# Kernel optimization log

Hardware: AMD Instinct MI355X
Metric: run time of the kernel (lower is better)

Reference implementation:

```python
import jax, jax.numpy as jnp
import numpy as np

D, M, B, K = 512, 128, 16, 4
COHERENCE_COEFF = 0.01
LAMBDA_COEFF = 1.0


def setup_inputs() -> dict:
    key = jax.random.key(0)
    k1, k2, k3, k4 = jax.random.split(key, 4)
    x = jax.random.normal(k1, (2, 2048, D), dtype=jnp.float32)
    V = jax.random.normal(k2, (D, M, B), dtype=jnp.float32)
    U = jax.random.normal(k3, (M, D, B), dtype=jnp.float32)
    u_scales = jax.random.normal(k4, (M, B), dtype=jnp.float32)
    return {"x": x, "V": V, "U": U, "u_scales": u_scales}


def _forward(x, V, U, u_scales):
    # UnitColNorm parametrizations: normalize over the D axis
    Vn = V / jnp.linalg.norm(V, axis=0, keepdims=True)          # (D, m, b)
    Un = U / jnp.linalg.norm(U, axis=1, keepdims=True)          # (m, D, b)
    s = jnp.tanh(u_scales) * LAMBDA_COEFF                        # (m, b)
    U_eff = Un * s[:, None, :]                                   # (m, D, b)

    expert_reprs = jnp.einsum('...d,dmb->...mb', x, Vn)          # (..., m, b)
    repr_l2_sq = jnp.sum(expert_reprs * expert_reprs, axis=-1)   # (..., m)
    topk_vals, topk_idxs = jax.lax.top_k(repr_l2_sq, K)          # (..., k)

    reprs_topk = jnp.take_along_axis(expert_reprs, topk_idxs[..., None], axis=-2)  # (..., k, b)
    U_active = U_eff[topk_idxs]                                  # (..., k, D, b)
    writes = jnp.einsum('...kdb,...kb->...d', U_active, reprs_topk)

    # aux terms
    N = topk_vals.size // K
    idxs_flat = topk_idxs.reshape(-1)
    vals_flat = topk_vals.reshape(-1)
    energy_per_expert = jnp.zeros((M,), dtype=vals_flat.dtype).at[idxs_flat].add(vals_flat) / N
    select_rate = jnp.zeros((M,), dtype=vals_flat.dtype).at[idxs_flat].add(1.0) / N
    total_energy = jnp.maximum(energy_per_expert.sum(), 1e-12)
    relative_energy = energy_per_expert / total_energy

    eye = jnp.eye(M * B, dtype=Vn.dtype)
    sqrtD = jnp.sqrt(jnp.asarray(D, dtype=Vn.dtype))

    def coherence_penalty(Mtx):
        G = Mtx.T @ Mtx  # (m*b, m*b)
        return jnp.abs(G - eye).mean() * sqrtD

    v_pen = coherence_penalty(Vn.reshape(D, M * B))
    u_pen = coherence_penalty(U_eff.transpose(1, 0, 2).reshape(D, M * B))
    aux_loss = COHERENCE_COEFF * v_pen - total_energy

    out = x + writes
    return (out, total_energy, energy_per_expert, relative_energy,
            select_rate, v_pen, u_pen, aux_loss)


def reference(x, V, U, u_scales):
    return _forward(x, V, U, u_scales)
```

## Files before the change

kernel.cpp:

```cpp
#include <hip/hip_runtime.h>
#include <math.h>

#define D 512
#define M 128
#define B 16
#define KSEL 4
#define NC 2048
#define NTOK 4096

typedef unsigned short ushort;
typedef unsigned int uint;
typedef unsigned long long u64;
typedef __attribute__((ext_vector_type(8))) short short8;
typedef __attribute__((ext_vector_type(4))) float floatx4;

#define WS_EACC   0
#define WS_CACC   128
#define WS_VSUM   256
#define WS_USUM   257
#define WS_CNT_I  258
#define WS_VSCALE 512
#define WS_USCALE 2560
#define WS_E_F    4608
#define WS_RBF_F  528896
#define WS_XH_F   2626048
#define WS_XL_F   3674624
#define WS_VHT_F  4723200
#define WS_VLT_F  5247488
#define WS_UHT_F  5771776
#define WS_ULT_F  6296064
#define WS_LIST_F 6820352

#define OUT_TE   2097152
#define OUT_EPE  2097153
#define OUT_RE   2097281
#define OUT_SR   2097409
#define OUT_VPEN 2097537
#define OUT_UPEN 2097538
#define OUT_AUX  2097539

#define GLDS16(g, l) __builtin_amdgcn_global_load_lds(                        \
    (const __attribute__((address_space(1))) unsigned int*)(g),               \
    (__attribute__((address_space(3))) unsigned int*)(l), 16, 0, 0)

__device__ __forceinline__ ushort f2bf(float f) {
    union { float f; uint u; } a; a.f = f;
    uint u = a.u;
    u += 0x7fffu + ((u >> 16) & 1u);
    return (ushort)(u >> 16);
}
__device__ __forceinline__ float bf2f(ushort h) {
    union { uint u; float f; } a; a.u = ((uint)h) << 16;
    return a.f;
}

__launch_bounds__(256)
__global__ void prep_kernel(const float* __restrict__ x, const float* __restrict__ V,
                            const float* __restrict__ U, const float* __restrict__ us_in,
                            ushort* __restrict__ xh, ushort* __restrict__ xl,
                            ushort* __restrict__ vht, ushort* __restrict__ vlt,
                            ushort* __restrict__ uht, ushort* __restrict__ ult,
                            float* __restrict__ ws) {
    __shared__ float ts[64][65];
    const int bid = blockIdx.x;
    const int tid = threadIdx.x;

    if (bid < 1024) {
        const int idx = (bid * 256 + tid) * 8;
        float4 v0 = *(const float4*)(x + idx);
        float4 v1 = *(const float4*)(x + idx + 4);
        float vv[8] = {v0.x, v0.y, v0.z, v0.w, v1.x, v1.y, v1.z, v1.w};
        union { ushort u[8]; uint4 q; } H, L;
#pragma unroll
        for (int j = 0; j < 8; ++j) {
            ushort h = f2bf(vv[j]);
            H.u[j] = h;
            L.u[j] = f2bf(vv[j] - bf2f(h));
        }
        *(uint4*)(xh + idx) = H.q;
        *(uint4*)(xl + idx) = L.q;
    } else if (bid < 1280) {
        const int vb = bid - 1024;
        const int col0 = (vb & 31) * 64;
        const int d0 = (vb >> 5) * 64;
#pragma unroll
        for (int i = 0; i < 16; ++i) {
            int idx = i * 256 + tid;
            int r = idx >> 6, c = idx & 63;
            ts[r][c] = V[(size_t)(d0 + r) * NC + col0 + c];
        }
        __syncthreads();
#pragma unroll
        for (int i = 0; i < 16; ++i) {
            int idx = i * 256 + tid;
            int c2 = idx >> 6, d2 = idx & 63;
            float v = ts[d2][c2];
            ushort h = f2bf(v);
            vht[(size_t)(col0 + c2) * D + d0 + d2] = h;
            vlt[(size_t)(col0 + c2) * D + d0 + d2] = f2bf(v - bf2f(h));
        }
    } else if (bid < 1408) {
        const int m = bid - 1280;
        float (*t2)[129] = (float (*)[129])ts;
        for (int d0 = 0; d0 < D; d0 += 128) {
            __syncthreads();
#pragma unroll
            for (int i = 0; i < 8; ++i) {
                int idx = i * 256 + tid;
                int d2 = idx >> 4, b2 = idx & 15;
                t2[b2][d2] = U[(size_t)m * (D * B) + (size_t)(d0 + d2) * B + b2];
            }
            __syncthreads();
#pragma unroll
            for (int i = 0; i < 8; ++i) {
                int idx = i * 256 + tid;
                int b3 = idx >> 7, d3 = idx & 127;
                float v = t2[b3][d3];
                ushort h = f2bf(v);
                uht[(size_t)((m << 4) + b3) * D + d0 + d3] = h;
                ult[(size_t)((m << 4) + b3) * D + d0 + d3] = f2bf(v - bf2f(h));
            }
        }
    } else {
        const int bx = bid - 1408;
        if (bx >= 160) {
            ws[(bx - 160) * 256 + tid] = 0.0f;
            return;
        }
        if (bx < 32) {
            const int c = bx * 64 + (tid & 63);
            const int dg = tid >> 6;
            float s = 0.0f;
            for (int d = dg; d < D; d += 4) {
                float v = V[(size_t)d * NC + c];
                s = fmaf(v, v, s);
            }
            float (*sh)[64] = (float (*)[64])ts;
            sh[dg][tid & 63] = s;
            __syncthreads();
            if (tid < 64) {
                float t = (sh[0][tid] + sh[1][tid]) + (sh[2][tid] + sh[3][tid]);
                ws[WS_VSCALE + bx * 64 + tid] = 1.0f / sqrtf(t);
            }
        } else {
            const int m = bx - 32;
            const float* p = U + (size_t)m * (D * B);
            float s = 0.0f;
            for (int i = tid; i < D * B; i += 256) {
                float v = p[i];
                s = fmaf(v, v, s);
            }
            float* sh2 = &ts[0][0];
            sh2[tid] = s;
            __syncthreads();
            if (tid < 16) {
                float t = 0.0f;
#pragma unroll
                for (int j = 0; j < 16; ++j) t += sh2[tid + (j << 4)];
                ws[WS_USCALE + (m << 4) + tid] = tanhf(us_in[(m << 4) + tid]) / sqrtf(t);
            }
        }
    }
}

__launch_bounds__(256)
__global__ void mfma_fused(const ushort* __restrict__ xh, const ushort* __restrict__ xl,
                           const ushort* __restrict__ vht, const ushort* __restrict__ vlt,
                           const ushort* __restrict__ uht, const ushort* __restrict__ ult,
                           float* __restrict__ ws, ushort* __restrict__ rbf) {
    __shared__ ushort smem[16384];
    const int bid = blockIdx.x;
    const int tid = threadIdx.x, lane = tid & 63, w = tid >> 6;
    const int wr = w >> 1, wc = w & 1;
    const int r15 = lane & 15, q = lane >> 4;
    const int srl = lane >> 2;
    const int skq = (lane & 3) ^ ((lane >> 3) & 3);
    const int perm8 = (q ^ ((r15 >> 1) & 3)) * 8;

    const int is_gemm = bid < 512;
    const ushort* srcs[4];
    int rbase[4];
    int gi = 0, gj = 0, which = 0;
    if (is_gemm) {
        const int x = bid & 7, inner = bid >> 3;
        const int tokG = ((x >> 1) << 3) + (inner & 7);
        const int colG = ((x & 1) << 3) + (inner >> 3);
        const int tokB = tokG * 128, colB = colG * 128;
        srcs[0] = xh; srcs[1] = xl; srcs[2] = vht; srcs[3] = vlt;
        rbase[0] = tokB; rbase[1] = tokB; rbase[2] = colB; rbase[3] = colB;
    } else {
        int t = bid - 512;
        which = t >= 136;
        if (which) t -= 136;
        int bi = 0, rem = 16;
        while (t >= rem) { t -= rem; --rem; ++bi; }
        gi = bi; gj = bi + t;
        const ushort* ht = which ? uht : vht;
        srcs[0] = ht; srcs[1] = ht; srcs[2] = ht; srcs[3] = ht;
        rbase[0] = gi * 128; rbase[1] = gi * 128; rbase[2] = gj * 128; rbase[3] = gj * 128;
    }

    floatx4 acc[4][4];
#pragma unroll
    for (int i = 0; i < 4; ++i)
#pragma unroll
        for (int j = 0; j < 4; ++j) acc[i][j] = (floatx4){0.f, 0.f, 0.f, 0.f};

    auto stage = [&](int c) {
        const int kb = c * 32 + skq * 8;
#pragma unroll
        for (int tI = 0; tI < 4; ++tI) {
            if (!is_gemm && (tI & 1)) continue;
            const ushort* s = srcs[tI] + (size_t)rbase[tI] * D + kb;
#pragma unroll
            for (int sub = 0; sub < 2; ++sub) {
                const int row16 = w * 32 + sub * 16;
                GLDS16(s + (size_t)(row16 + srl) * D,
                       &smem[tI * 4096 + row16 * 32]);
            }
        }
    };

    stage(0);
    for (int c = 0; c < 16; ++c) {
        __syncthreads();
        short8 ah[4], al[4], bh[4], bl[4];
#pragma unroll
        for (int s = 0; s < 4; ++s) {
            const int ra = (wr * 64 + s * 16 + r15) * 32 + perm8;
            ah[s] = *(const short8*)&smem[ra];
            const int rb = (wc * 64 + s * 16 + r15) * 32 + perm8;
            bh[s] = *(const short8*)&smem[8192 + rb];
            if (is_gemm) {
                al[s] = *(const short8*)&smem[4096 + ra];
                bl[s] = *(const short8*)&smem[12288 + rb];
            }
        }
        __syncthreads();
        if (c < 15) stage(c + 1);
#pragma unroll
        for (int st = 0; st < 4; ++st)
#pragma unroll
            for (int sc = 0; sc < 4; ++sc) {
                acc[st][sc] = __builtin_amdgcn_mfma_f32_16x16x32_bf16(ah[st], bh[sc], acc[st][sc], 0, 0, 0);
                if (is_gemm) {
                    acc[st][sc] = __builtin_amdgcn_mfma_f32_16x16x32_bf16(ah[st], bl[sc], acc[st][sc], 0, 0, 0);
                    acc[st][sc] = __builtin_amdgcn_mfma_f32_16x16x32_bf16(al[st], bh[sc], acc[st][sc], 0, 0, 0);
                }
            }
    }

    if (is_gemm) {
        const int tok0 = rbase[0] + wr * 64, col0 = rbase[2] + wc * 64;
        const int cg4 = col0 >> 6;
        float* e2base = ws + WS_E_F + (size_t)cg4 * (NTOK * 4);
#pragma unroll
        for (int st = 0; st < 4; ++st) {
            const int rowb = tok0 + st * 16 + q * 4;
            float er[4][4];
#pragma unroll
            for (int sc = 0; sc < 4; ++sc) {
                const int colg = col0 + sc * 16 + r15;
                const float vs = ws[WS_VSCALE + colg];
                float r0 = acc[st][sc][0] * vs;
                float r1 = acc[st][sc][1] * vs;
                float r2 = acc[st][sc][2] * vs;
                float r3 = acc[st][sc][3] * vs;
                rbf[(size_t)(rowb + 0) * NC + colg] = f2bf(r0);
                rbf[(size_t)(rowb + 1) * NC + colg] = f2bf(r1);
                rbf[(size_t)(rowb + 2) * NC + colg] = f2bf(r2);
                rbf[(size_t)(rowb + 3) * NC + colg] = f2bf(r3);
                float e0 = r0 * r0, e1 = r1 * r1, e2 = r2 * r2, e3 = r3 * r3;
#pragma unroll
                for (int mk = 1; mk < 16; mk <<= 1) {
                    e0 += __shfl_xor(e0, mk);
                    e1 += __shfl_xor(e1, mk);
                    e2 += __shfl_xor(e2, mk);
                    e3 += __shfl_xor(e3, mk);
                }
                er[sc][0] = e0; er[sc][1] = e1; er[sc][2] = e2; er[sc][3] = e3;
            }
            if (r15 == 0) {
#pragma unroll
                for (int j = 0; j < 4; ++j) {
                    *(float4*)(e2base + (size_t)(rowb + j) * 4) =
                        make_float4(er[0][j], er[1][j], er[2][j], er[3][j]);
                }
            }
        }
    } else {
        const float* scl = ws + (which ? WS_USCALE : WS_VSCALE);
        float* sum_out = ws + (which ? WS_USUM : WS_VSUM);
        float local = 0.0f;
#pragma unroll
        for (int sc = 0; sc < 4; ++sc) {
            const int colg = gj * 128 + wc * 64 + sc * 16 + r15;
            const float scj = scl[colg];
#pragma unroll
            for (int st = 0; st < 4; ++st) {
#pragma unroll
                for (int reg = 0; reg < 4; ++reg) {
                    const int rowg = gi * 128 + wr * 64 + st * 16 + q * 4 + reg;
                    float g = acc[st][sc][reg] * scl[rowg] * scj;
                    if (rowg == colg) g -= 1.0f;
                    local += fabsf(g);
                }
            }
        }
        if (gi < gj) local *= 2.0f;
#pragma unroll
        for (int mk = 1; mk < 64; mk <<= 1) local += __shfl_xor(local, mk);
        __shared__ float red[4];
        if (lane == 0) red[w] = local;
        __syncthreads();
        if (tid == 0) atomicAdd(sum_out, (red[0] + red[1]) + (red[2] + red[3]));
    }
}

__launch_bounds__(256)
__global__ void topk_kernel(float* __restrict__ ws) {
    const int tid = threadIdx.x, lane = tid & 63, w = tid >> 6;
    const int t = blockIdx.x * 4 + w;
    int* icnt = (int*)ws + WS_CNT_I;
    int* ilist = (int*)(ws + WS_LIST_F);

    const int cg4 = lane >> 1;
    const int e2off = (lane & 1) * 2;
    const float2 ev = *(const float2*)(ws + WS_E_F +
                                       ((size_t)cg4 * NTOK + t) * 4 + e2off);
    const uint i0 = (uint)(lane * 2), i1 = i0 + 1;
    u64 k0 = ((u64)__float_as_uint(ev.x) << 32) | (uint)(~i0);
    u64 k1 = ((u64)__float_as_uint(ev.y) << 32) | (uint)(~i1);
    u64 s0 = k0 > k1 ? k0 : k1;
    u64 s1 = k0 > k1 ? k1 : k0;
    u64 s2 = 0, s3 = 0;

#pragma unroll
    for (int mk = 1; mk < 64; mk <<= 1) {
        u64 o0 = __shfl_xor(s0, mk);
        u64 o1 = __shfl_xor(s1, mk);
        u64 o2 = __shfl_xor(s2, mk);
        u64 o3 = __shfl_xor(s3, mk);
        u64 c0 = s0 > o3 ? s0 : o3;
        u64 c1 = s1 > o2 ? s1 : o2;
        u64 c2 = s2 > o1 ? s2 : o1;
        u64 c3 = s3 > o0 ? s3 : o0;
        u64 d0 = c0 > c2 ? c0 : c2, d2 = c0 > c2 ? c2 : c0;
        u64 d1 = c1 > c3 ? c1 : c3, d3 = c1 > c3 ? c3 : c1;
        s0 = d0 > d1 ? d0 : d1; s1 = d0 > d1 ? d1 : d0;
        s2 = d2 > d3 ? d2 : d3; s3 = d2 > d3 ? d3 : d2;
    }

    if (lane < 4) {
        u64 key = (lane == 0) ? s0 : (lane == 1) ? s1 : (lane == 2) ? s2 : s3;
        const int e = (int)(~(uint)key);
        const float val = __uint_as_float((uint)(key >> 32));
        atomicAdd(&ws[WS_EACC + e], val);
        atomicAdd(&ws[WS_CACC + e], 1.0f);
        int pos = atomicAdd(&icnt[e], 1);
        ilist[(e << 12) + pos] = (t << 2) | lane;
    }
}

__launch_bounds__(256)
__global__ void expert_contrib_kernel(const float* __restrict__ U,
                                      const ushort* __restrict__ rbf,
                                      const float* __restrict__ ws,
                                      uint* __restrict__ contrib) {
    const int e = blockIdx.x;
    const int tid = threadIdx.x;
    const int cnt = ((const int*)ws)[WS_CNT_I + e];
    if ((int)blockIdx.y >= cnt) return;

    float usc[16];
#pragma unroll
    for (int b = 0; b < 16; ++b) usc[b] = ws[WS_USCALE + (e << 4) + b];

    const float* Up = U + (size_t)e * (D * B);
    float u0[16], u1[16];
#pragma unroll
    for (int qd = 0; qd < 4; ++qd) {
        float4 a = *(const float4*)(Up + (size_t)(2 * tid) * B + qd * 4);
        float4 b4 = *(const float4*)(Up + (size_t)(2 * tid + 1) * B + qd * 4);
        u0[qd * 4 + 0] = a.x * usc[qd * 4 + 0];
        u0[qd * 4 + 1] = a.y * usc[qd * 4 + 1];
        u0[qd * 4 + 2] = a.z * usc[qd * 4 + 2];
        u0[qd * 4 + 3] = a.w * usc[qd * 4 + 3];
        u1[qd * 4 + 0] = b4.x * usc[qd * 4 + 0];
        u1[qd * 4 + 1] = b4.y * usc[qd * 4 + 1];
        u1[qd * 4 + 2] = b4.z * usc[qd * 4 + 2];
        u1[qd * 4 + 3] = b4.w * usc[qd * 4 + 3];
    }

    const int* ilist = (const int*)(ws + WS_LIST_F) + (e << 12);
    int i = blockIdx.y;
    int pk = (i < cnt) ? ilist[i] : 0;
    while (i < cnt) {
        const int t = pk >> 2, k = pk & 3;
        const ushort* rp = rbf + (size_t)t * NC + (e << 4);
        union { ushort u[16]; uint4 q[2]; } R;
        R.q[0] = *(const uint4*)(rp);
        R.q[1] = *(const uint4*)(rp + 8);
        const int inext = i + 4;
        if (inext < cnt) pk = ilist[inext];
        float acc0 = 0.0f, acc1 = 0.0f;
#pragma unroll
        for (int b = 0; b < 16; ++b) {
            const float wv = bf2f(R.u[b]);
            acc0 = fmaf(u0[b], wv, acc0);
            acc1 = fmaf(u1[b], wv, acc1);
        }
        contrib[(size_t)((t << 2) + k) * 256 + tid] =
            (uint)f2bf(acc0) | ((uint)f2bf(acc1) << 16);
        i = inext;
    }
}

__launch_bounds__(256)
__global__ void combine_kernel(const float* __restrict__ x,
                               const uint* __restrict__ contrib,
                               const float* __restrict__ ws,
                               float* __restrict__ out) {
    if (blockIdx.x == 1024) {
        const int m = threadIdx.x;
        if (m >= 128) return;
        float e = ws[WS_EACC + m] * (1.0f / (float)NTOK);
        float c = ws[WS_CACC + m] * (1.0f / (float)NTOK);
        float s = e;
#pragma unroll
        for (int off = 32; off > 0; off >>= 1) s += __shfl_down(s, off);
        __shared__ float sh[2];
        if ((m & 63) == 0) sh[m >> 6] = s;
        __syncthreads();
        float total = sh[0] + sh[1];
        float total_energy = fmaxf(total, 1e-12f);
        out[OUT_EPE + m] = e;
        out[OUT_RE + m] = e / total_energy;
        out[OUT_SR + m] = c;
        if (m == 0) {
            out[OUT_TE] = total_energy;
            float inv_n2 = 1.0f / ((float)NC * (float)NC);
            float sqrtD = sqrtf((float)D);
            float vpen = ws[WS_VSUM] * inv_n2 * sqrtD;
            float upen = ws[WS_USUM] * inv_n2 * sqrtD;
            out[OUT_VPEN] = vpen;
            out[OUT_UPEN] = upen;
            out[OUT_AUX] = 0.01f * vpen - total_energy;
        }
        return;
    }

    const int gid = blockIdx.x * 256 + threadIdx.x;
    const int t = gid >> 6;
    const int dq = (gid & 63) << 3;
    const uint4* cp = (const uint4*)contrib;

    float s[8];
    float4 x0 = *(const float4*)(x + (size_t)t * D + dq);
    float4 x1 = *(const float4*)(x + (size_t)t * D + dq + 4);
    s[0] = x0.x; s[1] = x0.y; s[2] = x0.z; s[3] = x0.w;
    s[4] = x1.x; s[5] = x1.y; s[6] = x1.z; s[7] = x1.w;
#pragma unroll
    for (int k = 0; k < KSEL; ++k) {
        uint4 cvec = cp[(size_t)((t << 2) + k) * 64 + (dq >> 3)];
        uint cc[4] = {cvec.x, cvec.y, cvec.z, cvec.w};
#pragma unroll
        for (int j = 0; j < 4; ++j) {
            s[2 * j]     += bf2f((ushort)(cc[j] & 0xffffu));
            s[2 * j + 1] += bf2f((ushort)(cc[j] >> 16));
        }
    }
    float* op = out + (size_t)t * D + dq;
    *(float4*)(op)     = make_float4(s[0], s[1], s[2], s[3]);
    *(float4*)(op + 4) = make_float4(s[4], s[5], s[6], s[7]);
}

extern "C" void kernel_launch(void* const* d_in, const int* in_sizes, int n_in,
                              void* d_out, int out_size, void* d_ws, size_t ws_size,
                              hipStream_t stream) {
    const float* x  = (const float*)d_in[0];
    const float* V  = (const float*)d_in[1];
    const float* U  = (const float*)d_in[2];
    const float* us = (const float*)d_in[3];
    float* out = (float*)d_out;
    float* ws  = (float*)d_ws;

    ushort* xh  = (ushort*)(ws + WS_XH_F);
    ushort* xl  = (ushort*)(ws + WS_XL_F);
    ushort* vht = (ushort*)(ws + WS_VHT_F);
    ushort* vlt = (ushort*)(ws + WS_VLT_F);
    ushort* uht = (ushort*)(ws + WS_UHT_F);
    ushort* ult = (ushort*)(ws + WS_ULT_F);
    ushort* rbf = (ushort*)(ws + WS_RBF_F);
    uint* contrib = (uint*)(ws + WS_XH_F);

    prep_kernel<<<1570, 256, 0, stream>>>(x, V, U, us, xh, xl, vht, vlt, uht, ult, ws);
    mfma_fused<<<784, 256, 0, stream>>>(xh, xl, vht, vlt, uht, ult, ws, rbf);
    topk_kernel<<<NTOK / 4, 256, 0, stream>>>(ws);
    expert_contrib_kernel<<<dim3(128, 4), 256, 0, stream>>>(U, rbf, ws, contrib);
    combine_kernel<<<1025, 256, 0, stream>>>(x, contrib, ws, out);
}
```

Measured before the change: 193.7 us.

## Replace atomic per-expert list building with deterministic scan-based listbuild kernel

The top-k kernel now writes a packed selection record (value, expert, slot) per token-slot instead of doing three global atomics per selection. A new per-expert kernel scans all 16K records, counts matches with a block prefix sum, writes ordered index lists, and reduces energy and count sums. This removes atomic contention on hot experts and makes list order deterministic, at the cost of an extra launch and every expert block reading the full selection array.

```diff
diff --git a/kernel.cpp b/kernel.cpp
--- a/kernel.cpp
+++ b/kernel.cpp
@@ -30,6 +30,7 @@
 #define WS_UHT_F  5771776
 #define WS_ULT_F  6296064
 #define WS_LIST_F 6820352
+#define WS_SEL_F  7344640
 
 #define OUT_TE   2097152
 #define OUT_EPE  2097153
@@ -321,8 +322,6 @@
 __global__ void topk_kernel(float* __restrict__ ws) {
     const int tid = threadIdx.x, lane = tid & 63, w = tid >> 6;
     const int t = blockIdx.x * 4 + w;
-    int* icnt = (int*)ws + WS_CNT_I;
-    int* ilist = (int*)(ws + WS_LIST_F);
 
     const int cg4 = lane >> 1;
     const int e2off = (lane & 1) * 2;
@@ -353,12 +352,68 @@
 
     if (lane < 4) {
         u64 key = (lane == 0) ? s0 : (lane == 1) ? s1 : (lane == 2) ? s2 : s3;
-        const int e = (int)(~(uint)key);
-        const float val = __uint_as_float((uint)(key >> 32));
-        atomicAdd(&ws[WS_EACC + e], val);
-        atomicAdd(&ws[WS_CACC + e], 1.0f);
-        int pos = atomicAdd(&icnt[e], 1);
-        ilist[(e << 12) + pos] = (t << 2) | lane;
+        const uint e = (uint)(~(uint)key) & 127u;
+        const u64 lo = ((u64)(e << 14)) | (u64)((t << 2) | lane);
+        ((u64*)(ws + WS_SEL_F))[(t << 2) + lane] =
+            (key & 0xFFFFFFFF00000000ull) | lo;
+    }
+}
+
+__launch_bounds__(256)
+__global__ void listbuild_kernel(float* __restrict__ ws) {
+    const int e = blockIdx.x;
+    const int tid = threadIdx.x;
+    const u64* sels = (const u64*)(ws + WS_SEL_F);
+    int* icnt = (int*)ws + WS_CNT_I;
+    int* ilist = (int*)(ws + WS_LIST_F) + (e << 12);
+
+    __shared__ int sc_[256];
+    __shared__ float sv[256];
+
+    const int base_idx = tid * 64;
+    int cnt = 0;
+    float vsum = 0.0f;
+#pragma unroll 8
+    for (int j = 0; j < 64; ++j) {
+        u64 s = sels[base_idx + j];
+        if ((int)((s >> 14) & 127u) == e) {
+            ++cnt;
+            vsum += __uint_as_float((uint)(s >> 32));
+        }
+    }
+    sc_[tid] = cnt;
+    sv[tid] = vsum;
+    __syncthreads();
+
+#pragma unroll
+    for (int off = 1; off < 256; off <<= 1) {
+        int v = (tid >= off) ? sc_[tid - off] : 0;
+        __syncthreads();
+        sc_[tid] += v;
+        __syncthreads();
+    }
+    const int wbase = sc_[tid] - cnt;
+    const int total = sc_[255];
+
+    if (cnt > 0) {
+        int p = wbase;
+#pragma unroll 8
+        for (int j = 0; j < 64; ++j) {
+            u64 s = sels[base_idx + j];
+            if ((int)((s >> 14) & 127u) == e)
+                ilist[p++] = (int)(s & 0x3FFFu);
+        }
+    }
+
+#pragma unroll
+    for (int off = 128; off > 0; off >>= 1) {
+        __syncthreads();
+        if (tid < off) sv[tid] += sv[tid + off];
+    }
+    if (tid == 0) {
+        icnt[e] = total;
+        ws[WS_EACC + e] = sv[0];
+        ws[WS_CACC + e] = (float)total;
     }
 }
 
@@ -497,6 +552,7 @@
     prep_kernel<<<1570, 256, 0, stream>>>(x, V, U, us, xh, xl, vht, vlt, uht, ult, ws);
     mfma_fused<<<784, 256, 0, stream>>>(xh, xl, vht, vlt, uht, ult, ws, rbf);
     topk_kernel<<<NTOK / 4, 256, 0, stream>>>(ws);
+    listbuild_kernel<<<M, 256, 0, stream>>>(ws);
     expert_contrib_kernel<<<dim3(128, 4), 256, 0, stream>>>(U, rbf, ws, contrib);
     combine_kernel<<<1025, 256, 0, stream>>>(x, contrib, ws, out);
 }
```

New measurement: 168.4 us. 13.0% less time.
